# Optimization experiments

Measured on AMD Instinct MI355X. Metric: run time of the kernel, lower is better.

Reference implementation:

```python
import jax, jax.numpy as jnp
import numpy as np

IGNORE_INDEX = -100
LABEL_SMOOTHING = 0.0
LSE_SQUARE_SCALE = 0.0

N_TOKENS, HIDDEN, VOCAB = 4096, 2048, 32000


def setup_inputs() -> dict:
    key = jax.random.key(0)
    k1, k2, k3, k4 = jax.random.split(key, 4)
    lin_weight = jax.random.normal(k1, (VOCAB, HIDDEN), dtype=jnp.float32) * 0.02
    _input = jax.random.normal(k2, (N_TOKENS, HIDDEN), dtype=jnp.float32)
    target = jax.random.randint(k3, (N_TOKENS,), 0, VOCAB, dtype=jnp.int64)
    bias = jax.random.normal(k4, (VOCAB,), dtype=jnp.float32) * 0.02
    return {"lin_weight": lin_weight, "_input": _input, "target": target, "bias": bias}


def reference(lin_weight, _input, target, bias):
    # logits = _input @ lin_weight.T + bias : [N, V]
    logits = jnp.einsum("nh,vh->nv", _input, lin_weight) + bias[None, :]
    lse = jax.nn.logsumexp(logits, axis=-1)            # [N]
    valid = target != IGNORE_INDEX                      # [N] bool
    safe_tgt = jnp.where(valid, target, 0)
    x_t = jnp.take_along_axis(logits, safe_tgt[:, None], axis=-1)[:, 0]
    nll = lse - x_t                                     # per-token NLL
    eps = LABEL_SMOOTHING
    # label-smoothed CE: lse - (1-eps)*x_t - eps*mean(logits)
    smooth = lse - jnp.mean(logits, axis=-1)
    loss_i = (1.0 - eps) * nll + eps * smooth + LSE_SQUARE_SCALE * lse * lse
    loss_i = jnp.where(valid, loss_i, 0.0)
    n_valid = jnp.maximum(jnp.sum(valid), 1).astype(loss_i.dtype)
    return jnp.sum(loss_i) / n_valid  # reduction='mean' over non-ignored tokens
```

## Files before the change

kernel.cpp:

```cpp
#include <hip/hip_runtime.h>
#include <hip/hip_bf16.h>
#include <stdint.h>

#define IGNORE_INDEX (-100)

typedef float f32x4 __attribute__((ext_vector_type(4)));
typedef int i32x4 __attribute__((ext_vector_type(4)));

constexpr int NTOK = 4096;
constexpr int HID  = 2048;
constexpr int VOC  = 32000;
constexpr int BM = 128, BN = 128, BKB = 64;
constexpr int NT_N = VOC / BN;
constexpr int NT_M = NTOK / BM;
constexpr int KSTEPS = HID / 64;

#define XSCALE 16.0f
#define WSCALE 1024.0f
#define INV_SCALE (1.0f / 16384.0f)


__device__ __forceinline__ unsigned q8(float v, float s) {
  int q = __float2int_rn(v * s);
  q = max(-127, min(127, q));
  return (unsigned)(q & 0xff);
}

__device__ __forceinline__ unsigned pack4(float4 a, float s) {
  return q8(a.x, s) | (q8(a.y, s) << 8) | (q8(a.z, s) << 16) | (q8(a.w, s) << 24);
}

__global__ void cvti8_kernel(const float* __restrict__ src, uint2* __restrict__ dst,
                             size_t n8, float scale) {
  size_t i = (size_t)blockIdx.x * blockDim.x + threadIdx.x;
  size_t stride = (size_t)gridDim.x * blockDim.x;
  const float4* s4 = reinterpret_cast<const float4*>(src);
  for (; i < n8; i += stride) {
    float4 a = s4[2 * i];
    float4 b = s4[2 * i + 1];
    dst[i] = make_uint2(pack4(a, scale), pack4(b, scale));
  }
}

__global__ void cvtfrag_kernel(const float* __restrict__ src, uint4* __restrict__ dst,
                               int nrows, float scale) {
  int u = blockIdx.x * blockDim.x + threadIdx.x;
  int total = nrows * 128;
  int stride = gridDim.x * blockDim.x;
  const float4* s4 = reinterpret_cast<const float4*>(src);
  for (; u < total; u += stride) {
    int row = u >> 7;
    int kc = u & 127;
    const float4* p = s4 + ((size_t)row * 512 + kc * 4);
    float4 a = p[0], b = p[1], c = p[2], d = p[3];
    uint4 o;
    o.x = pack4(a, scale); o.y = pack4(b, scale);
    o.z = pack4(c, scale); o.w = pack4(d, scale);
    size_t fi = ((size_t)(row >> 4) * KSTEPS + (kc >> 2)) * 64 + (kc & 3) * 16 + (row & 15);
    dst[fi] = o;
  }
}

__global__ void xt_kernel(const float* __restrict__ X, const float* __restrict__ W,
                          const float* __restrict__ bias, const int* __restrict__ tgt,
                          float* __restrict__ xt) {
  int row = blockIdx.x * 4 + (threadIdx.x >> 6);
  int lane = threadIdx.x & 63;
  if (row >= NTOK) return;
  int t = tgt[row];
  if (t < 0 || t >= VOC) { if (lane == 0) xt[row] = 0.0f; return; }
  const float4* xr = reinterpret_cast<const float4*>(X + (size_t)row * HID);
  const float4* wr = reinterpret_cast<const float4*>(W + (size_t)t * HID);
  float s = 0.0f;
  for (int i = lane; i < HID / 4; i += 64) {
    float4 a = xr[i], b = wr[i];
    s += a.x * b.x + a.y * b.y + a.z * b.z + a.w * b.w;
  }
#pragma unroll
  for (int d = 1; d < 64; d <<= 1) s += __shfl_xor(s, d);
  if (lane == 0) xt[row] = s + bias[t];
}

__global__ __launch_bounds__(256, 4) void gemm_lse_kernel(
    const uint8_t* __restrict__ Xf, const uint8_t* __restrict__ Wi8,
    const float* __restrict__ bias,
    float* __restrict__ pmax, float* __restrict__ psum) {
  __shared__ __align__(16) uint8_t Bs[BN * BKB];
  __shared__ float redM[2][BM];
  __shared__ float redS[2][BM];

  const int nwg = NT_M * NT_N;
  const int xcd = blockIdx.x & 7;
  const int pos = blockIdx.x >> 3;
  const int wgid = xcd * (nwg >> 3) + pos;
  const int mtile = wgid & (NT_M - 1);
  const int ntile = wgid >> 5;
  const int mbase = mtile * BM;
  const int nbase = ntile * BN;

  const int tid = threadIdx.x;
  const int w = tid >> 6;
  const int lane = tid & 63;
  const int wr = w >> 1, wc = w & 1;
  const int l15 = lane & 15;
  const int kgrp = lane >> 4;

  const int srow = tid >> 2;
  const int csrc = (tid & 3) ^ ((tid >> 3) & 3);
  const uint8_t* bSt0 = Wi8 + (size_t)(nbase + srow) * HID + csrc * 16;
  const uint8_t* bSt1 = bSt0 + (size_t)64 * HID;

  const int swz16 = (kgrp ^ ((l15 >> 1) & 3)) * 16;
  const int brow0 = wc * 64 + l15;

  const int lofs = kgrp * 256 + l15 * 16;
  const uint8_t* aP[4];
#pragma unroll
  for (int mi = 0; mi < 4; ++mi)
    aP[mi] = Xf + ((size_t)((mbase >> 4) + wr * 4 + mi) * KSTEPS) * 1024 + lofs;

  i32x4 acc[4][4];
#pragma unroll
  for (int mi = 0; mi < 4; ++mi)
#pragma unroll
    for (int ni = 0; ni < 4; ++ni)
#pragma unroll
      for (int j = 0; j < 4; ++j) acc[mi][ni][j] = 0;

  float bv[4];
#pragma unroll
  for (int ni = 0; ni < 4; ++ni) bv[ni] = bias[nbase + wc * 64 + ni * 16 + l15];

#define GLDS(SRC, DST)                                                              \
  __builtin_amdgcn_global_load_lds((const __attribute__((address_space(1))) void*)(SRC), \
                                   (__attribute__((address_space(3))) void*)(DST), 16, 0, 0)

  for (int t = 0; t < KSTEPS; ++t) {
    __syncthreads();
    GLDS(bSt0 + t * 64, Bs + tid * 16);
    GLDS(bSt1 + t * 64, Bs + 4096 + tid * 16);
    i32x4 af[4];
#pragma unroll
    for (int mi = 0; mi < 4; ++mi)
      af[mi] = *reinterpret_cast<const i32x4*>(aP[mi] + (size_t)t * 1024);
    __syncthreads();

    i32x4 bg[4];
#pragma unroll
    for (int ni = 0; ni < 4; ++ni)
      bg[ni] = *reinterpret_cast<const i32x4*>(Bs + (brow0 + ni * 16) * BKB + swz16);
#pragma unroll
    for (int mi = 0; mi < 4; ++mi)
#pragma unroll
      for (int ni = 0; ni < 4; ++ni)
        acc[mi][ni] = __builtin_amdgcn_mfma_i32_16x16x64_i8(
            af[mi], bg[ni], acc[mi][ni], 0, 0, 0);
  }
#undef GLDS

#pragma unroll
  for (int mi = 0; mi < 4; ++mi) {
#pragma unroll
    for (int j = 0; j < 4; ++j) {
      float v0 = fmaf((float)acc[mi][0][j], INV_SCALE, bv[0]);
      float v1 = fmaf((float)acc[mi][1][j], INV_SCALE, bv[1]);
      float v2 = fmaf((float)acc[mi][2][j], INV_SCALE, bv[2]);
      float v3 = fmaf((float)acc[mi][3][j], INV_SCALE, bv[3]);
      float mx = fmaxf(fmaxf(v0, v1), fmaxf(v2, v3));
#pragma unroll
      for (int d = 1; d < 16; d <<= 1) mx = fmaxf(mx, __shfl_xor(mx, d));
      float s = __expf(v0 - mx) + __expf(v1 - mx) + __expf(v2 - mx) + __expf(v3 - mx);
#pragma unroll
      for (int d = 1; d < 16; d <<= 1) s += __shfl_xor(s, d);
      if (l15 == 0) {
        int lr = wr * 64 + mi * 16 + kgrp * 4 + j;
        redM[wc][lr] = mx;
        redS[wc][lr] = s;
      }
    }
  }
  __syncthreads();
  if (tid < BM) {
    float m0 = redM[0][tid], m1 = redM[1][tid];
    float M = fmaxf(m0, m1);
    float S = __expf(m0 - M) * redS[0][tid] + __expf(m1 - M) * redS[1][tid];
    size_t row = (size_t)mbase + tid;
    pmax[(size_t)ntile * NTOK + row] = M;
    psum[(size_t)ntile * NTOK + row] = S;
  }
}

__global__ void lse_kernel(const float* __restrict__ pmax, const float* __restrict__ psum,
                           const float* __restrict__ xt, const int* __restrict__ tgt,
                           float* __restrict__ loss) {
  int row = blockIdx.x * 4 + (threadIdx.x >> 6);
  int lane = threadIdx.x & 63;
  if (row >= NTOK) return;
  float M = -3.4e38f;
  for (int i = lane; i < NT_N; i += 64) M = fmaxf(M, pmax[(size_t)i * NTOK + row]);
#pragma unroll
  for (int d = 1; d < 64; d <<= 1) M = fmaxf(M, __shfl_xor(M, d));
  float S = 0.0f;
  for (int i = lane; i < NT_N; i += 64)
    S += __expf(pmax[(size_t)i * NTOK + row] - M) * psum[(size_t)i * NTOK + row];
#pragma unroll
  for (int d = 1; d < 64; d <<= 1) S += __shfl_xor(S, d);
  if (lane == 0) {
    int tg = tgt[row];
    bool valid = (tg != IGNORE_INDEX);
    float lse = M + __logf(S);
    loss[row] = valid ? (lse - xt[row]) : 0.0f;
  }
}

__global__ void final_kernel(const float* __restrict__ loss, const int* __restrict__ tgt,
                             float* __restrict__ out) {
  __shared__ float shs[256];
  __shared__ float shc[256];
  int tid = threadIdx.x;
  float s = 0.0f, c = 0.0f;
  for (int i = tid; i < NTOK; i += 256) {
    s += loss[i];
    c += (tgt[i] != IGNORE_INDEX) ? 1.0f : 0.0f;
  }
  shs[tid] = s; shc[tid] = c;
  __syncthreads();
  for (int off = 128; off > 0; off >>= 1) {
    if (tid < off) { shs[tid] += shs[tid + off]; shc[tid] += shc[tid + off]; }
    __syncthreads();
  }
  if (tid == 0) out[0] = shs[0] / fmaxf(shc[0], 1.0f);
}

extern "C" void kernel_launch(void* const* d_in, const int* in_sizes, int n_in,
                              void* d_out, int out_size, void* d_ws, size_t ws_size,
                              hipStream_t stream) {
  const float* W    = (const float*)d_in[0];
  const float* X    = (const float*)d_in[1];
  const int*   tgt  = (const int*)d_in[2];
  const float* bias = (const float*)d_in[3];
  float* out = (float*)d_out;

  char* ws = (char*)d_ws;
  uint8_t* Wi8 = (uint8_t*)(ws);
  uint8_t* Xf  = (uint8_t*)(ws + 65536000);
  float* pmax  = (float*)  (ws + 73924608);
  float* psum  = (float*)  (ws + 78020608);
  float* xt    = (float*)  (ws + 82116608);
  float* loss  = (float*)  (ws + 82132992);

  cvti8_kernel<<<2048, 256, 0, stream>>>(W, (uint2*)Wi8, (size_t)VOC * HID / 8, WSCALE);
  cvtfrag_kernel<<<1024, 256, 0, stream>>>(X, (uint4*)Xf, NTOK, XSCALE);
  xt_kernel<<<NTOK / 4, 256, 0, stream>>>(X, W, bias, tgt, xt);
  gemm_lse_kernel<<<NT_M * NT_N, 256, 0, stream>>>(Xf, Wi8, bias, pmax, psum);
  lse_kernel<<<NTOK / 4, 256, 0, stream>>>(pmax, psum, xt, tgt, loss);
  final_kernel<<<1, 256, 0, stream>>>(loss, tgt, out);
}
```

Baseline: 426.3 us.

## Double-buffer B tile in LDS and prefetch A fragments one K-step ahead

Converts the K loop of the int8 GEMM+LSE kernel into a software pipeline. The B slab is double-buffered in LDS and the next step's global_load_lds is issued before the current MFMAs. A fragments for the next step are prefetched with inline-asm loads into alternating register sets. Manual vmcnt waits and one barrier per step replace the two syncthreads per iteration, aiming to hide global load latency behind the MFMAs. The cost is more LDS and registers, plus fragile hand-counted waitcnt values that may interact with compiler-generated loads.

```diff
diff --git a/kernel.cpp b/kernel.cpp
--- a/kernel.cpp
+++ b/kernel.cpp
@@ -85,7 +85,7 @@
     const uint8_t* __restrict__ Xf, const uint8_t* __restrict__ Wi8,
     const float* __restrict__ bias,
     float* __restrict__ pmax, float* __restrict__ psum) {
-  __shared__ __align__(16) uint8_t Bs[BN * BKB];
+  __shared__ __align__(16) uint8_t Bs[2][BN * BKB];
   __shared__ float redM[2][BM];
   __shared__ float redS[2][BM];
 
@@ -114,10 +114,10 @@
   const int brow0 = wc * 64 + l15;
 
   const int lofs = kgrp * 256 + l15 * 16;
-  const uint8_t* aP[4];
-#pragma unroll
-  for (int mi = 0; mi < 4; ++mi)
-    aP[mi] = Xf + ((size_t)((mbase >> 4) + wr * 4 + mi) * KSTEPS) * 1024 + lofs;
+  const uint8_t* aQ0 = Xf + ((size_t)((mbase >> 4) + wr * 4 + 0) * KSTEPS) * 1024 + lofs;
+  const uint8_t* aQ1 = Xf + ((size_t)((mbase >> 4) + wr * 4 + 1) * KSTEPS) * 1024 + lofs;
+  const uint8_t* aQ2 = Xf + ((size_t)((mbase >> 4) + wr * 4 + 2) * KSTEPS) * 1024 + lofs;
+  const uint8_t* aQ3 = Xf + ((size_t)((mbase >> 4) + wr * 4 + 3) * KSTEPS) * 1024 + lofs;
 
   i32x4 acc[4][4];
 #pragma unroll
@@ -134,28 +134,63 @@
 #define GLDS(SRC, DST)                                                              \
   __builtin_amdgcn_global_load_lds((const __attribute__((address_space(1))) void*)(SRC), \
                                    (__attribute__((address_space(3))) void*)(DST), 16, 0, 0)
-
-  for (int t = 0; t < KSTEPS; ++t) {
-    __syncthreads();
-    GLDS(bSt0 + t * 64, Bs + tid * 16);
-    GLDS(bSt1 + t * 64, Bs + 4096 + tid * 16);
-    i32x4 af[4];
-#pragma unroll
-    for (int mi = 0; mi < 4; ++mi)
-      af[mi] = *reinterpret_cast<const i32x4*>(aP[mi] + (size_t)t * 1024);
-    __syncthreads();
-
+#define STAGE_B(TK, SLAB)                                                           \
+  { GLDS(bSt0 + (TK) * 64, &Bs[(SLAB)][tid * 16]);                                  \
+    GLDS(bSt1 + (TK) * 64, &Bs[(SLAB)][4096 + tid * 16]); }
+#define ALOAD4(AF, TK)                                                              \
+  { asm volatile("global_load_dwordx4 %0, %1, off" : "=v"(AF[0]) : "v"(aQ0 + (size_t)(TK) * 1024)); \
+    asm volatile("global_load_dwordx4 %0, %1, off" : "=v"(AF[1]) : "v"(aQ1 + (size_t)(TK) * 1024)); \
+    asm volatile("global_load_dwordx4 %0, %1, off" : "=v"(AF[2]) : "v"(aQ2 + (size_t)(TK) * 1024)); \
+    asm volatile("global_load_dwordx4 %0, %1, off" : "=v"(AF[3]) : "v"(aQ3 + (size_t)(TK) * 1024)); }
+#define BREAD(BG, SLAB)                                                             \
+  _Pragma("unroll")                                                                 \
+  for (int ni = 0; ni < 4; ++ni)                                                    \
+    BG[ni] = *reinterpret_cast<const i32x4*>(&Bs[(SLAB)][(brow0 + ni * 16) * BKB + swz16]);
+#define MFMA16(AF, BG)                                                              \
+  _Pragma("unroll")                                                                 \
+  for (int mi = 0; mi < 4; ++mi)                                                    \
+    _Pragma("unroll")                                                               \
+    for (int ni = 0; ni < 4; ++ni)                                                  \
+      acc[mi][ni] = __builtin_amdgcn_mfma_i32_16x16x64_i8(AF[mi], BG[ni],           \
+                                                          acc[mi][ni], 0, 0, 0);
+#define BODY(T, SLABC, SLABN, AFC, AFN)                                             \
+  { STAGE_B((T) + 1, SLABN)                                                         \
+    i32x4 bg[4];                                                                    \
+    BREAD(bg, SLABC)                                                                \
+    ALOAD4(AFN, (T) + 1)                                                            \
+    asm volatile("s_waitcnt vmcnt(6)" ::: "memory");                                \
+    __builtin_amdgcn_sched_barrier(0);                                              \
+    MFMA16(AFC, bg)                                                                 \
+    __builtin_amdgcn_sched_barrier(0);                                              \
+    asm volatile("s_waitcnt vmcnt(4)" ::: "memory");                                \
+    __builtin_amdgcn_s_barrier();                                                   \
+    asm volatile("" ::: "memory"); }
+
+  i32x4 afE[4], afO[4];
+  STAGE_B(0, 0)
+  ALOAD4(afE, 0)
+  asm volatile("s_waitcnt vmcnt(0)" ::: "memory");
+  __builtin_amdgcn_s_barrier();
+  asm volatile("" ::: "memory");
+
+  for (int tt = 0; tt < KSTEPS - 2; tt += 2) {
+    BODY(tt,     0, 1, afE, afO)
+    BODY(tt + 1, 1, 0, afO, afE)
+  }
+  BODY(KSTEPS - 2, 0, 1, afE, afO)
+  {
     i32x4 bg[4];
-#pragma unroll
-    for (int ni = 0; ni < 4; ++ni)
-      bg[ni] = *reinterpret_cast<const i32x4*>(Bs + (brow0 + ni * 16) * BKB + swz16);
-#pragma unroll
-    for (int mi = 0; mi < 4; ++mi)
-#pragma unroll
-      for (int ni = 0; ni < 4; ++ni)
-        acc[mi][ni] = __builtin_amdgcn_mfma_i32_16x16x64_i8(
-            af[mi], bg[ni], acc[mi][ni], 0, 0, 0);
-  }
+    BREAD(bg, 1)
+    asm volatile("s_waitcnt vmcnt(0)" ::: "memory");
+    __builtin_amdgcn_sched_barrier(0);
+    MFMA16(afO, bg)
+  }
+
+#undef BODY
+#undef MFMA16
+#undef BREAD
+#undef ALOAD4
+#undef STAGE_B
 #undef GLDS
 
 #pragma unroll
```

Result: slower. 514.3 us (+20.6%).
